# Optimization experiments

Hardware: AMD Instinct MI355X
Metric: run time of the kernel (lower is better)

The kernel has to match this reference:

```python
import jax, jax.numpy as jnp
import numpy as np

N_NODES = 100000
N_EDGES = 1600000
D_IN = 128
D_OUT = 128


def setup_inputs() -> dict:
    key = jax.random.key(0)
    ks = jax.random.split(key, 8)
    h = jax.random.normal(ks[0], (N_NODES, D_IN), dtype=jnp.float32)
    edge_val = jax.random.uniform(ks[1], (N_EDGES,), dtype=jnp.float32)
    # Linear weights in torch layout [out, in]
    W_self = jax.random.normal(ks[2], (D_OUT, D_IN), dtype=jnp.float32) * (1.0 / np.sqrt(D_IN))
    b_self = jax.random.normal(ks[3], (D_OUT,), dtype=jnp.float32) * 0.01
    W_nb = jax.random.normal(ks[4], (D_OUT, D_IN), dtype=jnp.float32) * (1.0 / np.sqrt(D_IN))
    b_nb = jax.random.normal(ks[5], (D_OUT,), dtype=jnp.float32) * 0.01
    edge_row = jax.random.randint(ks[6], (N_EDGES,), 0, N_NODES, dtype=jnp.int64)
    edge_col = jax.random.randint(ks[7], (N_EDGES,), 0, N_NODES, dtype=jnp.int64)
    return {"h": h, "edge_val": edge_val, "W_self": W_self, "b_self": b_self,
            "W_nb": W_nb, "b_nb": b_nb, "edge_row": edge_row, "edge_col": edge_col}


def reference(h, edge_val, W_self, b_self, W_nb, b_nb, edge_row, edge_col):
    # self_h = Linear_self(h[:out_nodes]); out_nodes == N_NODES here
    self_h = h @ W_self.T + b_self  # [N, D_OUT]
    # neighbor_h = adj.spmm(h): sparse COO (row, col, val) times dense h
    msgs = edge_val[:, None] * h[edge_col]            # [E, D_IN]
    neighbor_h = jax.ops.segment_sum(msgs, edge_row, num_segments=N_NODES)  # [N, D_IN]
    out = self_h + neighbor_h @ W_nb.T + b_nb
    return out
```

## Files before the change

kernel.cpp:

```cpp
#include <hip/hip_runtime.h>


constexpr int NN = 100000;
constexpr int NE = 1600000;
constexpr int D  = 128;
constexpr int NN_PAD = 100032;
constexpr int NBUCK  = 391;
constexpr int BCAP   = 4608;
constexpr int CHUNK  = 4096;
constexpr int NCH    = (NE + CHUNK - 1) / CHUNK;

typedef __bf16 bf16x8 __attribute__((ext_vector_type(8)));
typedef float  f32x4  __attribute__((ext_vector_type(4)));

__global__ __launch_bounds__(256) void w_convert(
    const float* __restrict__ Wself, const float* __restrict__ Wnb,
    __bf16* __restrict__ wcat) {
    int i = blockIdx.x * 256 + threadIdx.x;
    int n = i >> 7, k = i & 127;
    float v = (n < D) ? Wself[(size_t)n * D + k] : Wnb[(size_t)(n - D) * D + k];
    wcat[i] = (__bf16)v;
}

__global__ __launch_bounds__(256) void gemm_mfma(
    const float* __restrict__ h,
    const __bf16* __restrict__ wcat,
    const float* __restrict__ bself,
    const float* __restrict__ bnb,
    float* __restrict__ out,
    __bf16* __restrict__ tmpb)
{
    const int t    = threadIdx.x;
    const int w    = t >> 6;
    const int lane = t & 63;
    const int l15  = lane & 15;
    const int quad = lane >> 4;

    bf16x8 b[4][4];
    #pragma unroll
    for (int ns = 0; ns < 4; ++ns) {
        const __bf16* wb = wcat + (size_t)(w * 64 + ns * 16 + l15) * D + quad * 8;
        #pragma unroll
        for (int kk = 0; kk < 4; ++kk)
            b[ns][kk] = *(const bf16x8*)(wb + kk * 32);
    }

    float bias[4];
    #pragma unroll
    for (int ns = 0; ns < 4; ++ns) {
        int col = w * 64 + ns * 16 + l15;
        bias[ns] = (col < D) ? (bself[col] + bnb[col]) : 0.f;
    }

    #pragma unroll
    for (int c = 0; c < 4; ++c) {
        const int m0 = blockIdx.x * 64 + c * 16;
        int arow = m0 + l15;
        if (arow >= NN) arow = NN - 1;
        const float* aptr = h + (size_t)arow * D + quad * 8;

        bf16x8 afr[4];
        #pragma unroll
        for (int kk = 0; kk < 4; ++kk) {
            f32x4 lo = *(const f32x4*)(aptr + kk * 32);
            f32x4 hi = *(const f32x4*)(aptr + kk * 32 + 4);
            bf16x8 a;
            #pragma unroll
            for (int j = 0; j < 4; ++j) { a[j] = (__bf16)lo[j]; a[4 + j] = (__bf16)hi[j]; }
            afr[kk] = a;
        }

        f32x4 acc[4];
        #pragma unroll
        for (int ns = 0; ns < 4; ++ns) acc[ns] = (f32x4){0.f, 0.f, 0.f, 0.f};
        #pragma unroll
        for (int ns = 0; ns < 4; ++ns)
            #pragma unroll
            for (int kk = 0; kk < 4; ++kk)
                acc[ns] = __builtin_amdgcn_mfma_f32_16x16x32_bf16(afr[kk], b[ns][kk], acc[ns], 0, 0, 0);

        if (w < 2) {
            #pragma unroll
            for (int ns = 0; ns < 4; ++ns) {
                int col = w * 64 + ns * 16 + l15;
                #pragma unroll
                for (int i = 0; i < 4; ++i) {
                    int row = m0 + quad * 4 + i;
                    if (row < NN) out[(size_t)row * D + col] = acc[ns][i] + bias[ns];
                }
            }
        } else {
            #pragma unroll
            for (int ns = 0; ns < 4; ++ns) {
                int col = w * 64 + ns * 16 + l15 - D;
                #pragma unroll
                for (int i = 0; i < 4; ++i) {
                    int row = m0 + quad * 4 + i;
                    if (row < NN) tmpb[(size_t)row * D + col] = (__bf16)acc[ns][i];
                }
            }
        }
    }
}

__global__ __launch_bounds__(256) void wc_scatter(
    const int* __restrict__ erow, const int* __restrict__ ecol,
    const float* __restrict__ eval_,
    int* __restrict__ gcount, int2* __restrict__ epair)
{
    __shared__ int  cnt[NBUCK];
    __shared__ int  lscan[NBUCK];
    __shared__ int  gbase[NBUCK];
    __shared__ int  ss[512];
    __shared__ int2 sbuf[CHUNK];
    __shared__ int  saddr[CHUNK];
    __shared__ int  s_total;

    const int t  = threadIdx.x;
    const int c0 = blockIdx.x * CHUNK;

    for (int b = t; b < NBUCK; b += 256) cnt[b] = 0;
    __syncthreads();

    int   bp[16];
    int   colr[16];
    float valr[16];
    #pragma unroll
    for (int j = 0; j < 16; ++j) {
        int e = c0 + j * 256 + t;
        if (e < NE) {
            int r   = erow[e];
            colr[j] = ecol[e];
            valr[j] = eval_[e];
            int b   = r >> 8;
            int pos = atomicAdd(&cnt[b], 1);
            bp[j]   = b | ((r & 255) << 9) | (pos << 17);
        } else bp[j] = -1;
    }
    __syncthreads();

    ss[t]       = (t < NBUCK)       ? cnt[t]       : 0;
    ss[t + 256] = (t + 256 < NBUCK) ? cnt[t + 256] : 0;
    __syncthreads();
    for (int off = 1; off < 512; off <<= 1) {
        int i0 = t, i1 = t + 256;
        int r0 = ss[i0] + ((i0 >= off) ? ss[i0 - off] : 0);
        int r1 = ss[i1] + ((i1 >= off) ? ss[i1 - off] : 0);
        __syncthreads();
        ss[i0] = r0; ss[i1] = r1;
        __syncthreads();
    }
    if (t < NBUCK) {
        int n = cnt[t];
        lscan[t] = ss[t] - n;
        gbase[t] = (n > 0) ? atomicAdd(&gcount[t], n) : 0;
    }
    if (t + 256 < NBUCK) {
        int n = cnt[t + 256];
        lscan[t + 256] = ss[t + 256] - n;
        gbase[t + 256] = (n > 0) ? atomicAdd(&gcount[t + 256], n) : 0;
    }
    if (t == 0) s_total = ss[511];
    __syncthreads();

    #pragma unroll
    for (int j = 0; j < 16; ++j) {
        if (bp[j] >= 0) {
            int b   = bp[j] & 511;
            int rlo = (bp[j] >> 9) & 255;
            int pos = bp[j] >> 17;
            int slot = lscan[b] + pos;
            sbuf[slot]  = make_int2(colr[j] | (rlo << 17), __float_as_int(valr[j]));
            saddr[slot] = b * BCAP + gbase[b] + pos;
        }
    }
    __syncthreads();

    int ce = s_total;
    for (int i = t; i < ce; i += 256)
        epair[saddr[i]] = sbuf[i];
}

__global__ __launch_bounds__(256) void bucket_sort(
    const int2* __restrict__ epair, const int* __restrict__ gcount,
    int2* __restrict__ epair2, int2* __restrict__ rowrange)
{
    __shared__ int  cnt[256];
    __shared__ int  off[256];
    __shared__ int  cur[256];
    __shared__ int  ss[256];
    __shared__ int2 sorted[BCAP];

    const int t = threadIdx.x;
    const int b = blockIdx.x;
    const int n = gcount[b];
    const int2* src = epair + (size_t)b * BCAP;

    cnt[t] = 0;
    __syncthreads();
    for (int i = t; i < n; i += 256)
        atomicAdd(&cnt[(src[i].x >> 17) & 255], 1);
    __syncthreads();

    int v = cnt[t];
    ss[t] = v;
    __syncthreads();
    for (int o = 1; o < 256; o <<= 1) {
        int y = (t >= o) ? ss[t - o] : 0;
        __syncthreads();
        ss[t] += y;
        __syncthreads();
    }
    off[t] = ss[t] - v;
    cur[t] = ss[t] - v;
    __syncthreads();

    for (int i = t; i < n; i += 256) {
        int2 p = src[i];
        int slot = atomicAdd(&cur[(p.x >> 17) & 255], 1);
        sorted[slot] = p;
    }
    __syncthreads();

    const int base = b * BCAP;
    for (int i = t; i < n; i += 256)
        epair2[base + i] = sorted[i];
    int row = b * 256 + t;
    if (row < NN)
        rowrange[row] = make_int2(base + off[t], base + off[t] + cnt[t]);
}

__global__ __launch_bounds__(256) void aggregate(
    const __bf16* __restrict__ tmpb, const int2* __restrict__ rowrange,
    const int2* __restrict__ epair2, float* __restrict__ out)
{
    int wave = (blockIdx.x * 256 + threadIdx.x) >> 6;
    if (wave >= NN) return;
    int lane = threadIdx.x & 63;
    int2 rr = rowrange[wave];
    int beg = rr.x, end = rr.y;

    float ax[4] = {0.f, 0.f, 0.f, 0.f};
    float ay[4] = {0.f, 0.f, 0.f, 0.f};
    int e = beg;
    for (; e + 7 < end; e += 8) {
        int2 p[8];
        #pragma unroll
        for (int k = 0; k < 8; ++k) p[k] = epair2[e + k];
        unsigned u[8];
        #pragma unroll
        for (int k = 0; k < 8; ++k) {
            int col = p[k].x & 0x1FFFF;
            u[k] = *(const unsigned*)(tmpb + (size_t)col * D + lane * 2);
        }
        #pragma unroll
        for (int k = 0; k < 8; ++k) {
            float v = __int_as_float(p[k].y);
            ax[k & 3] += v * __uint_as_float(u[k] << 16);
            ay[k & 3] += v * __uint_as_float(u[k] & 0xffff0000u);
        }
    }
    for (; e < end; ++e) {
        int2 p = epair2[e];
        int col = p.x & 0x1FFFF;
        unsigned u = *(const unsigned*)(tmpb + (size_t)col * D + lane * 2);
        float v = __int_as_float(p.y);
        ax[0] += v * __uint_as_float(u << 16);
        ay[0] += v * __uint_as_float(u & 0xffff0000u);
    }
    float2* o = (float2*)(out + (size_t)wave * D + lane * 2);
    float2 c = *o;
    c.x += (ax[0] + ax[1]) + (ax[2] + ax[3]);
    c.y += (ay[0] + ay[1]) + (ay[2] + ay[3]);
    *o = c;
}

extern "C" void kernel_launch(void* const* d_in, const int* in_sizes, int n_in,
                              void* d_out, int out_size, void* d_ws, size_t ws_size,
                              hipStream_t stream) {
    const float* h     = (const float*)d_in[0];
    const float* eval_ = (const float*)d_in[1];
    const float* Wself = (const float*)d_in[2];
    const float* bself = (const float*)d_in[3];
    const float* Wnb   = (const float*)d_in[4];
    const float* bnb   = (const float*)d_in[5];
    const int*   erow  = (const int*)d_in[6];
    const int*   ecol  = (const int*)d_in[7];
    float* out = (float*)d_out;

    char* p = (char*)d_ws;
    __bf16* tmpb    = (__bf16*)p;   p += (size_t)NN_PAD * D * 2;
    int2*   epair   = (int2*)p;     p += (size_t)NBUCK * BCAP * 8;
    int2*   epair2  = (int2*)p;     p += (size_t)NBUCK * BCAP * 8;
    int2*   rowrange= (int2*)p;     p += (size_t)NN * 8;
    __bf16* wcat    = (__bf16*)p;   p += 256 * 128 * 2;
    int*    gcount  = (int*)p;

    hipMemsetAsync(gcount, 0, NBUCK * 4, stream);

    w_convert<<<128, 256, 0, stream>>>(Wself, Wnb, wcat);
    gemm_mfma<<<NN_PAD / 64, 256, 0, stream>>>(h, wcat, bself, bnb, out, tmpb);
    wc_scatter<<<NCH, 256, 0, stream>>>(erow, ecol, eval_, gcount, epair);
    bucket_sort<<<NBUCK, 256, 0, stream>>>(epair, gcount, epair2, rowrange);
    aggregate<<<(NN * 64) / 256, 256, 0, stream>>>(tmpb, rowrange, epair2, out);
}
```

Before: 284.7 us.

## Fold weight conversion into GEMM and retune aggregate kernel loads and launches

Result: faster. 278.5 us (-2.2%).

```diff
diff --git a/kernel.cpp b/kernel.cpp
--- a/kernel.cpp
+++ b/kernel.cpp
@@ -12,19 +12,12 @@
 
 typedef __bf16 bf16x8 __attribute__((ext_vector_type(8)));
 typedef float  f32x4  __attribute__((ext_vector_type(4)));
-
-__global__ __launch_bounds__(256) void w_convert(
-    const float* __restrict__ Wself, const float* __restrict__ Wnb,
-    __bf16* __restrict__ wcat) {
-    int i = blockIdx.x * 256 + threadIdx.x;
-    int n = i >> 7, k = i & 127;
-    float v = (n < D) ? Wself[(size_t)n * D + k] : Wnb[(size_t)(n - D) * D + k];
-    wcat[i] = (__bf16)v;
-}
+typedef float  f32x2  __attribute__((ext_vector_type(2)));
 
 __global__ __launch_bounds__(256) void gemm_mfma(
     const float* __restrict__ h,
-    const __bf16* __restrict__ wcat,
+    const float* __restrict__ Wself,
+    const float* __restrict__ Wnb,
     const float* __restrict__ bself,
     const float* __restrict__ bnb,
     float* __restrict__ out,
@@ -39,10 +32,18 @@
     bf16x8 b[4][4];
     #pragma unroll
     for (int ns = 0; ns < 4; ++ns) {
-        const __bf16* wb = wcat + (size_t)(w * 64 + ns * 16 + l15) * D + quad * 8;
-        #pragma unroll
-        for (int kk = 0; kk < 4; ++kk)
-            b[ns][kk] = *(const bf16x8*)(wb + kk * 32);
+        int wrow = w * 64 + ns * 16 + l15;
+        const float* wr = (wrow < D) ? (Wself + (size_t)wrow * D)
+                                     : (Wnb + (size_t)(wrow - D) * D);
+        #pragma unroll
+        for (int kk = 0; kk < 4; ++kk) {
+            f32x4 lo = *(const f32x4*)(wr + kk * 32 + quad * 8);
+            f32x4 hi = *(const f32x4*)(wr + kk * 32 + quad * 8 + 4);
+            bf16x8 bb;
+            #pragma unroll
+            for (int j = 0; j < 4; ++j) { bb[j] = (__bf16)lo[j]; bb[4 + j] = (__bf16)hi[j]; }
+            b[ns][kk] = bb;
+        }
     }
 
     float bias[4];
@@ -232,32 +233,30 @@
 
 __global__ __launch_bounds__(256) void aggregate(
     const __bf16* __restrict__ tmpb, const int2* __restrict__ rowrange,
-    const int2* __restrict__ epair2, float* __restrict__ out)
+    const int2* __restrict__ epair2, float* __restrict__ out,
+    int row0, int nrows)
 {
-    int wave = (blockIdx.x * 256 + threadIdx.x) >> 6;
-    if (wave >= NN) return;
+    int wave = row0 + ((blockIdx.x * 256 + threadIdx.x) >> 6);
+    if (wave >= row0 + nrows) return;
     int lane = threadIdx.x & 63;
     int2 rr = rowrange[wave];
-    int beg = rr.x, end = rr.y;
+    int beg = __builtin_amdgcn_readfirstlane(rr.x);
+    int end = __builtin_amdgcn_readfirstlane(rr.y);
 
     float ax[4] = {0.f, 0.f, 0.f, 0.f};
     float ay[4] = {0.f, 0.f, 0.f, 0.f};
     int e = beg;
-    for (; e + 7 < end; e += 8) {
-        int2 p[8];
-        #pragma unroll
-        for (int k = 0; k < 8; ++k) p[k] = epair2[e + k];
-        unsigned u[8];
-        #pragma unroll
-        for (int k = 0; k < 8; ++k) {
+    for (; e + 3 < end; e += 4) {
+        int2 p[4];
+        #pragma unroll
+        for (int k = 0; k < 4; ++k) p[k] = epair2[e + k];
+        #pragma unroll
+        for (int k = 0; k < 4; ++k) {
             int col = p[k].x & 0x1FFFF;
-            u[k] = *(const unsigned*)(tmpb + (size_t)col * D + lane * 2);
-        }
-        #pragma unroll
-        for (int k = 0; k < 8; ++k) {
+            unsigned u = *(const unsigned*)(tmpb + (size_t)col * D + lane * 2);
             float v = __int_as_float(p[k].y);
-            ax[k & 3] += v * __uint_as_float(u[k] << 16);
-            ay[k & 3] += v * __uint_as_float(u[k] & 0xffff0000u);
+            ax[k] += v * __uint_as_float(u << 16);
+            ay[k] += v * __uint_as_float(u & 0xffff0000u);
         }
     }
     for (; e < end; ++e) {
@@ -268,11 +267,11 @@
         ax[0] += v * __uint_as_float(u << 16);
         ay[0] += v * __uint_as_float(u & 0xffff0000u);
     }
-    float2* o = (float2*)(out + (size_t)wave * D + lane * 2);
-    float2 c = *o;
+    f32x2* o = (f32x2*)(out + (size_t)wave * D + lane * 2);
+    f32x2 c = __builtin_nontemporal_load(o);
     c.x += (ax[0] + ax[1]) + (ax[2] + ax[3]);
     c.y += (ay[0] + ay[1]) + (ay[2] + ay[3]);
-    *o = c;
+    __builtin_nontemporal_store(c, o);
 }
 
 extern "C" void kernel_launch(void* const* d_in, const int* in_sizes, int n_in,
@@ -293,14 +292,13 @@
     int2*   epair   = (int2*)p;     p += (size_t)NBUCK * BCAP * 8;
     int2*   epair2  = (int2*)p;     p += (size_t)NBUCK * BCAP * 8;
     int2*   rowrange= (int2*)p;     p += (size_t)NN * 8;
-    __bf16* wcat    = (__bf16*)p;   p += 256 * 128 * 2;
     int*    gcount  = (int*)p;
 
     hipMemsetAsync(gcount, 0, NBUCK * 4, stream);
 
-    w_convert<<<128, 256, 0, stream>>>(Wself, Wnb, wcat);
-    gemm_mfma<<<NN_PAD / 64, 256, 0, stream>>>(h, wcat, bself, bnb, out, tmpb);
+    gemm_mfma<<<NN_PAD / 64, 256, 0, stream>>>(h, Wself, Wnb, bself, bnb, out, tmpb);
     wc_scatter<<<NCH, 256, 0, stream>>>(erow, ecol, eval_, gcount, epair);
     bucket_sort<<<NBUCK, 256, 0, stream>>>(epair, gcount, epair2, rowrange);
-    aggregate<<<(NN * 64) / 256, 256, 0, stream>>>(tmpb, rowrange, epair2, out);
-}
+    aggregate<<<(50000 * 64) / 256, 256, 0, stream>>>(tmpb, rowrange, epair2, out, 0, 50000);
+    aggregate<<<(50000 * 64) / 256, 256, 0, stream>>>(tmpb, rowrange, epair2, out, 50000, 50000);
+}
```
